# Kernel tuning notes

Measured on AMD Instinct MI355X. Metric: run time of the kernel, lower is better.

## Reference

```python
import jax, jax.numpy as jnp
import numpy as np

B, T, S, NH, MD, FF, H = 2, 4096, 4096, 16, 64, 128, 4
HD = MD // H
NEG_SLOPE = 0.2
MAX_LOG_SCALE = float(np.log(100.0))  # SwinV2-style clamp on learnable logit scale


def layer_norm(x, g, b, eps=1e-5):
    mu = x.mean(-1, keepdims=True)
    var = ((x - mu) ** 2).mean(-1, keepdims=True)
    return (x - mu) * jax.lax.rsqrt(var + eps) * g + b


def leaky(x):
    return jnp.where(x >= 0, x, NEG_SLOPE * x)


def setup_inputs() -> dict:
    key = jax.random.key(0)
    ks = jax.random.split(key, 16)
    p = lambda i, shape: 0.02 * jax.random.normal(ks[i], shape, jnp.float32)
    return dict(
        x=jax.random.normal(ks[0], (B, S, 1), jnp.float32),
        coords_target=jax.random.uniform(ks[1], (B, T, 2), jnp.float32),
        coords_source=jax.random.uniform(ks[2], (B, S, 2), jnp.float32),
        pe_w1=p(3, (2, FF)), pe_b1=jnp.zeros((FF,), jnp.float32),
        pe_w2=p(4, (FF, MD)), pe_b2=jnp.zeros((MD,), jnp.float32),
        q_w=p(5, (MD, MD)), k_w=p(6, (MD, MD)), v_w=p(7, (1, MD)),
        logit_scale=jnp.zeros((H,), jnp.float32),
        out_w=p(8, (MD, MD)), out_b=jnp.zeros((MD,), jnp.float32),
        nh_w1=p(9, (MD, FF)), nh_b1=jnp.zeros((FF,), jnp.float32),
        nh_w2=p(10, (FF, 1)), nh_b2=jnp.zeros((1,), jnp.float32),
        uf_w1=p(11, (MD * NH, MD * NH)), uf_b1=jnp.zeros((MD * NH,), jnp.float32),
        uf_w2=p(12, (MD * NH, MD * NH)), uf_b2=jnp.zeros((MD * NH,), jnp.float32),
        ln1_g=jnp.ones((MD,), jnp.float32), ln1_b=jnp.zeros((MD,), jnp.float32),
        ln2_g=jnp.ones((MD,), jnp.float32), ln2_b=jnp.zeros((MD,), jnp.float32),
        ln3_g=jnp.ones((MD * NH,), jnp.float32), ln3_b=jnp.zeros((MD * NH,), jnp.float32),
    )


def reference(x, coords_target, coords_source, pe_w1, pe_b1, pe_w2, pe_b2,
              q_w, k_w, v_w, logit_scale, out_w, out_b,
              nh_w1, nh_b1, nh_w2, nh_b2, uf_w1, uf_b1, uf_w2, uf_b2,
              ln1_g, ln1_b, ln2_g, ln2_b, ln3_g, ln3_b):
    # ---- nn_layer: kNN gather of source values per target point ----
    d2 = jnp.sum((coords_target[:, :, None, :] - coords_source[:, None, :, :]) ** 2, -1)  # (B,T,S)
    _, idx = jax.lax.top_k(-d2, NH)  # (B,T,NH) nearest source indices
    gather = jax.vmap(lambda a, i: a[i])
    x_nh = gather(x, idx)                  # (B,T,NH,1)
    cs_nh = gather(coords_source, idx)     # (B,T,NH,2)
    rel = cs_nh - coords_target[:, :, None, :]  # relative coords (B,T,NH,2)

    # ---- relative position embedding MLP (with coordinate transform) ----
    c = jnp.sign(rel) * jnp.log1p(jnp.abs(rel))
    pe = jax.nn.relu(c @ pe_w1 + pe_b1) @ pe_w2 + pe_b2  # (B,T,NH,MD)

    # ---- value projection from raw gathered values (before pe add) ----
    v = x_nh.reshape(B * T, NH, 1) @ v_w  # (BT,NH,MD)

    h = layer_norm(x_nh + pe, ln1_g, ln1_b).reshape(B * T, NH, MD)
    q = h @ q_w
    k = h @ k_w

    # ---- local multi-head attention over the NH neighbors (cosine att w/ learnable logit scale) ----
    qh = q.reshape(B * T, NH, H, HD)
    kh = k.reshape(B * T, NH, H, HD)
    vh = v.reshape(B * T, NH, H, HD)
    qn = qh / (jnp.linalg.norm(qh, axis=-1, keepdims=True) + 1e-12)
    kn = kh / (jnp.linalg.norm(kh, axis=-1, keepdims=True) + 1e-12)
    scale = jnp.exp(jnp.minimum(logit_scale, MAX_LOG_SCALE))  # (H,)
    logits = jnp.einsum('nihd,njhd->nhij', qn, kn) * scale[None, :, None, None]
    att = jax.nn.softmax(logits, axis=-1)
    ao = jnp.einsum('nhij,njhd->nihd', att, vh).reshape(B * T, NH, MD)
    ao = ao @ out_w + out_b

    h = layer_norm(h + ao, ln2_g, ln2_b)
    # per-neighborhood MLP: md -> ff -> 1, broadcast residual add
    m = leaky(leaky(h @ nh_w1 + nh_b1) @ nh_w2 + nh_b2)  # (BT,NH,1)
    h = h + m

    # unfold neighbors into channel dim and run wide MLP
    hu = layer_norm(h.reshape(B, T, NH * MD), ln3_g, ln3_b)
    out = leaky(leaky(hu @ uf_w1 + uf_b1) @ uf_w2 + uf_b2)  # (B,T,NH*MD)
    return out
```

## Files before the change

### kernel.cpp

```cpp
#include <hip/hip_runtime.h>
#include <math.h>

#define B_ 2
#define T_ 4096
#define S_ 4096
#define NH_ 16
#define MD_ 64
#define FF_ 128
#define H_ 4
#define HD_ 16
#define BT_ (B_*T_)

typedef unsigned short u16;
typedef unsigned int u32;
typedef unsigned long long u64;
typedef __attribute__((ext_vector_type(8))) short short8;
typedef __attribute__((ext_vector_type(4))) float f32x4;

__device__ __forceinline__ float wsum64(float v) {
  #pragma unroll
  for (int off = 32; off > 0; off >>= 1) v += __shfl_xor(v, off, 64);
  return v;
}
__device__ __forceinline__ float leaky_(float x) { return x >= 0.f ? x : 0.2f * x; }
__device__ __forceinline__ u16 f2bf(float f) {
  u32 u = __float_as_uint(f);
  return (u16)((u + 0x7fffu + ((u >> 16) & 1u)) >> 16);
}
__device__ __forceinline__ float bf2f(u16 h) { return __uint_as_float((u32)h << 16); }

__device__ __forceinline__ void gload16(const void* g, void* l) {
  __builtin_amdgcn_global_load_lds(
      (const __attribute__((address_space(1))) u32*)g,
      (__attribute__((address_space(3))) u32*)l, 16, 0, 0);
}

__device__ __forceinline__ float dist2_(float2 c, float ctx, float cty) {
  float dx = ctx - c.x, dy = cty - c.y;
  return dx * dx + dy * dy;
}

__global__ __launch_bounds__(256) void k1_knn(
    const float* __restrict__ coords_target, const float* __restrict__ coords_source,
    const float* __restrict__ x, float* __restrict__ xnh, float* __restrict__ rel) {
  __shared__ float2 cs_s[S_];
  __shared__ u64 buf[4][128];
  const int tid = threadIdx.x;
  const int lane = tid & 63;
  const int wave = tid >> 6;
  const int n = blockIdx.x * 4 + wave;
  const int b = n >> 12;
  const float2* cs = (const float2*)coords_source + (size_t)b * S_;
  for (int i = tid; i < S_; i += 256) cs_s[i] = cs[i];
  __syncthreads();

  const float ctx = coords_target[n*2+0], cty = coords_target[n*2+1];

  float lmin = INFINITY;
  for (int kk = 0; kk < 64; ++kk)
    lmin = fminf(lmin, dist2_(cs_s[(kk << 6) | lane], ctx, cty));

  float v = lmin;
  #pragma unroll
  for (int k = 2; k <= 64; k <<= 1) {
    #pragma unroll
    for (int j = k >> 1; j > 0; j >>= 1) {
      float o = __shfl_xor(v, j, 64);
      bool keepmin = (((lane & j) == 0) == ((lane & k) == 0));
      v = keepmin ? fminf(v, o) : fmaxf(v, o);
    }
  }
  const float tau = __shfl(v, 15, 64);

  u64* wbuf = buf[wave];
  int cnt = 0;
  for (int kk = 0; kk < 64; ++kk) {
    int s = (kk << 6) | lane;
    float d2 = dist2_(cs_s[s], ctx, cty);
    bool q = (d2 <= tau);
    u64 mask = __ballot(q);
    if (q) {
      int pos = cnt + __popcll(mask & ((1ull << lane) - 1ull));
      if (pos < 128)
        wbuf[pos] = ((u64)__float_as_uint(d2) << 32) | (u32)s;
    }
    cnt += (int)__popcll(mask);
  }

  int myidx = 0;
  if (cnt >= 16 && cnt <= 128) {
    u64 c0 = (lane < cnt) ? wbuf[lane] : ~0ull;
    u64 c1 = (lane + 64 < cnt) ? wbuf[lane + 64] : ~0ull;
    for (int r = 0; r < 16; ++r) {
      u64 m = c0 < c1 ? c0 : c1;
      #pragma unroll
      for (int off = 32; off > 0; off >>= 1) {
        u64 o = __shfl_xor(m, off, 64);
        m = o < m ? o : m;
      }
      if (lane == r) myidx = (int)(u32)(m & 0xffffffffu);
      if (c0 == m) c0 = ~0ull;
      else if (c1 == m) c1 = ~0ull;
    }
  } else {
    float kd[16]; int ki[16];
    #pragma unroll
    for (int j = 0; j < 16; ++j) { kd[j] = INFINITY; ki[j] = 0x7fffffff; }
    for (int kk = 0; kk < 64; ++kk) {
      int s = (kk << 6) | lane;
      float d2 = dist2_(cs_s[s], ctx, cty);
      if (d2 < kd[15]) {
        float cd = d2; int ci = s;
        #pragma unroll
        for (int j = 0; j < 16; ++j) {
          bool sw = cd < kd[j];
          float td = sw ? kd[j] : cd;  int ti = sw ? ki[j] : ci;
          kd[j]    = sw ? cd : kd[j];  ki[j]    = sw ? ci : ki[j];
          cd = td; ci = ti;
        }
      }
    }
    for (int r = 0; r < 16; ++r) {
      float hd = kd[0]; int hi = ki[0];
      #pragma unroll
      for (int off = 32; off > 0; off >>= 1) {
        float od = __shfl_xor(hd, off, 64); int oi = __shfl_xor(hi, off, 64);
        bool take = (od < hd) || (od == hd && oi < hi);
        hd = take ? od : hd; hi = take ? oi : hi;
      }
      if (kd[0] == hd && ki[0] == hi) {
        #pragma unroll
        for (int j = 0; j < 15; ++j) { kd[j] = kd[j+1]; ki[j] = ki[j+1]; }
        kd[15] = INFINITY; ki[15] = 0x7fffffff;
      }
      if (lane == r) myidx = hi;
    }
  }

  if (lane < 16) {
    float2 c = cs_s[myidx];
    xnh[(size_t)n*NH_ + lane] = x[(size_t)b*S_ + myidx];
    rel[((size_t)n*NH_ + lane)*2 + 0] = c.x - ctx;
    rel[((size_t)n*NH_ + lane)*2 + 1] = c.y - cty;
  }
}

__global__ __launch_bounds__(256) void k2_pe(
    const float* __restrict__ rel, const float* __restrict__ xnh,
    const float* __restrict__ pe_w1, const float* __restrict__ pe_b1,
    const float* __restrict__ pe_w2, const float* __restrict__ pe_b2,
    const float* __restrict__ ln1_g, const float* __restrict__ ln1_b,
    float* __restrict__ h_out) {
  const int lane = threadIdx.x & 63;
  const int wave = threadIdx.x >> 6;
  __shared__ float hid[4][4][128];
  const int row0 = blockIdx.x * 16 + wave * 4;

  float c0[4], c1[4], xn[4];
  #pragma unroll
  for (int rr = 0; rr < 4; ++rr) {
    int row = row0 + rr;
    float r0 = rel[(size_t)row*2+0], r1 = rel[(size_t)row*2+1];
    float a0 = log1pf(fabsf(r0)), a1 = log1pf(fabsf(r1));
    c0[rr] = r0 > 0.f ? a0 : (r0 < 0.f ? -a0 : 0.f);
    c1[rr] = r1 > 0.f ? a1 : (r1 < 0.f ? -a1 : 0.f);
    xn[rr] = xnh[row];
  }
  const float w1a0 = pe_w1[lane],    w1a1 = pe_w1[128+lane], b1a = pe_b1[lane];
  const float w1b0 = pe_w1[64+lane], w1b1 = pe_w1[192+lane], b1b = pe_b1[64+lane];
  #pragma unroll
  for (int rr = 0; rr < 4; ++rr) {
    hid[wave][rr][lane]    = fmaxf(fmaf(c0[rr], w1a0, fmaf(c1[rr], w1a1, b1a)), 0.f);
    hid[wave][rr][lane+64] = fmaxf(fmaf(c0[rr], w1b0, fmaf(c1[rr], w1b1, b1b)), 0.f);
  }
  __syncthreads();

  const float b2 = pe_b2[lane];
  float acc[4] = {b2, b2, b2, b2};
  for (int j = 0; j < 128; ++j) {
    float w2 = pe_w2[(size_t)j*64 + lane];
    #pragma unroll
    for (int rr = 0; rr < 4; ++rr) acc[rr] = fmaf(hid[wave][rr][j], w2, acc[rr]);
  }

  const float g = ln1_g[lane], bb = ln1_b[lane];
  #pragma unroll
  for (int rr = 0; rr < 4; ++rr) {
    float v = xn[rr] + acc[rr];
    float mu = wsum64(v) * (1.f/64.f);
    float d = v - mu;
    float var = wsum64(d*d) * (1.f/64.f);
    h_out[(size_t)(row0+rr)*64 + lane] = d * rsqrtf(var + 1e-5f) * g + bb;
  }
}

#define HBF_S 72
#define QKS2 24
__global__ __launch_bounds__(256) void k3_attn(
    const float* __restrict__ h_in, const float* __restrict__ xnh,
    const u16* __restrict__ qkwt_hi, const u16* __restrict__ qkwt_lo,
    const u16* __restrict__ nhw1t_hi, const u16* __restrict__ nhw1t_lo,
    const float* __restrict__ v_w, const float* __restrict__ logit_scale,
    const float* __restrict__ out_w, const float* __restrict__ out_b,
    const float* __restrict__ nh_b1, const float* __restrict__ nh_w2,
    const float* __restrict__ nh_b2,
    const float* __restrict__ ln2_g, const float* __restrict__ ln2_b,
    const float* __restrict__ ln3_g, const float* __restrict__ ln3_b,
    u16* __restrict__ hu_hi, u16* __restrict__ hu_lo) {
  const int tid = threadIdx.x;
  const int lane = tid & 63;
  const int wave = tid >> 6;
  const int n = blockIdx.x * 4 + wave;

  __shared__ u16 h_bf[2][64][HBF_S];
  __shared__ u16 q_s[4][64][QKS2];
  __shared__ u16 k_s[4][64][QKS2];
  __shared__ float xnh_s[64];
  __shared__ float svx_s[4][16][4];
  __shared__ float mred[4][64];

  const float* hb = h_in + (size_t)n * (NH_*MD_);
  float hr[16];
  #pragma unroll
  for (int i = 0; i < 16; ++i) {
    hr[i] = hb[i*64 + lane];
    u16 hi16 = f2bf(hr[i]);
    h_bf[0][wave*16 + i][lane] = hi16;
    h_bf[1][wave*16 + i][lane] = f2bf(hr[i] - bf2f(hi16));
  }
  if (tid < 64) xnh_s[tid] = xnh[(size_t)blockIdx.x * 64 + tid];

  float wvo[4];
  #pragma unroll
  for (int h = 0; h < 4; ++h) {
    float a = 0.f;
    for (int d = 0; d < 16; ++d)
      a = fmaf(v_w[h*16+d], out_w[(size_t)(h*16+d)*64 + lane], a);
    wvo[h] = a;
  }
  __syncthreads();

  const int fr = lane & 15, fq = lane >> 4;
  {
    short8 bqh[2], bql[2], bkh[2], bkl[2];
    #pragma unroll
    for (int ks = 0; ks < 2; ++ks) {
      const int qcol = wave*16 + fr, kcol = 64 + wave*16 + fr;
      const int ko = ks*32 + fq*8;
      bqh[ks] = *(const short8*)&qkwt_hi[qcol*64 + ko];
      bql[ks] = *(const short8*)&qkwt_lo[qcol*64 + ko];
      bkh[ks] = *(const short8*)&qkwt_hi[kcol*64 + ko];
      bkl[ks] = *(const short8*)&qkwt_lo[kcol*64 + ko];
    }
    f32x4 accq[4], acck[4];
    #pragma unroll
    for (int mf = 0; mf < 4; ++mf) { accq[mf] = (f32x4){0,0,0,0}; acck[mf] = (f32x4){0,0,0,0}; }
    #pragma unroll
    for (int ks = 0; ks < 2; ++ks) {
      #pragma unroll
      for (int mf = 0; mf < 4; ++mf) {
        short8 ah = *(const short8*)&h_bf[0][mf*16 + fr][ks*32 + fq*8];
        short8 al = *(const short8*)&h_bf[1][mf*16 + fr][ks*32 + fq*8];
        accq[mf] = __builtin_amdgcn_mfma_f32_16x16x32_bf16(ah, bqh[ks], accq[mf], 0,0,0);
        accq[mf] = __builtin_amdgcn_mfma_f32_16x16x32_bf16(ah, bql[ks], accq[mf], 0,0,0);
        accq[mf] = __builtin_amdgcn_mfma_f32_16x16x32_bf16(al, bqh[ks], accq[mf], 0,0,0);
        acck[mf] = __builtin_amdgcn_mfma_f32_16x16x32_bf16(ah, bkh[ks], acck[mf], 0,0,0);
        acck[mf] = __builtin_amdgcn_mfma_f32_16x16x32_bf16(ah, bkl[ks], acck[mf], 0,0,0);
        acck[mf] = __builtin_amdgcn_mfma_f32_16x16x32_bf16(al, bkh[ks], acck[mf], 0,0,0);
      }
    }
    #pragma unroll
    for (int mf = 0; mf < 4; ++mf)
      #pragma unroll
      for (int r = 0; r < 4; ++r) {
        const int row = mf*16 + fq*4 + r;
        q_s[wave][row][fr] = f2bf(accq[mf][r]);
        k_s[wave][row][fr] = f2bf(acck[mf][r]);
      }
  }
  __syncthreads();

  {
    const int nl = lane >> 4, il = lane & 15;
    const float sc = expf(fminf(logit_scale[wave], 4.60517019f));
    float qv[16]; float qs = 0.f;
    short8 qp0 = *(const short8*)&q_s[wave][lane][0];
    short8 qp1 = *(const short8*)&q_s[wave][lane][8];
    #pragma unroll
    for (int d = 0; d < 8; ++d) {
      qv[d]   = bf2f((u16)qp0[d]);  qs = fmaf(qv[d],   qv[d],   qs);
      qv[8+d] = bf2f((u16)qp1[d]);  qs = fmaf(qv[8+d], qv[8+d], qs);
    }
    const float rq = 1.f / (sqrtf(qs) + 1e-12f);
    float lg[16];
    #pragma unroll
    for (int j = 0; j < 16; ++j) {
      short8 kp0 = *(const short8*)&k_s[wave][(lane & 48) + j][0];
      short8 kp1 = *(const short8*)&k_s[wave][(lane & 48) + j][8];
      float ks = 0.f, dt = 0.f;
      #pragma unroll
      for (int d = 0; d < 8; ++d) {
        float kv0 = bf2f((u16)kp0[d]);
        float kv1 = bf2f((u16)kp1[d]);
        ks = fmaf(kv0, kv0, ks); dt = fmaf(qv[d], kv0, dt);
        ks = fmaf(kv1, kv1, ks); dt = fmaf(qv[8+d], kv1, dt);
      }
      lg[j] = dt * rq * (1.f/(sqrtf(ks)+1e-12f)) * sc;
    }
    float mx = lg[0];
    #pragma unroll
    for (int j = 1; j < 16; ++j) mx = fmaxf(mx, lg[j]);
    float se = 0.f, sx = 0.f;
    #pragma unroll
    for (int j = 0; j < 16; ++j) {
      float e = __expf(lg[j] - mx);
      se += e;
      sx = fmaf(e, xnh_s[(lane & 48) + j], sx);
    }
    svx_s[nl][il][wave] = sx / se;
  }
  __syncthreads();

  const float ob = out_b[lane], g2 = ln2_g[lane], bb2 = ln2_b[lane];
  float h2[16];
  #pragma unroll
  for (int i = 0; i < 16; ++i) {
    float o = ob;
    #pragma unroll
    for (int h = 0; h < 4; ++h) o = fmaf(svx_s[wave][i][h], wvo[h], o);
    float t = hr[i] + o;
    float mu = wsum64(t) * (1.f/64.f);
    float d = t - mu;
    float var = wsum64(d*d) * (1.f/64.f);
    h2[i] = d * rsqrtf(var + 1e-5f) * g2 + bb2;
  }
  #pragma unroll
  for (int i = 0; i < 16; ++i) {
    u16 hi16 = f2bf(h2[i]);
    h_bf[0][wave*16 + i][lane] = hi16;
    h_bf[1][wave*16 + i][lane] = f2bf(h2[i] - bf2f(hi16));
  }
  __syncthreads();

  {
    short8 bnh[2][2], bnl[2][2];
    float b1v[2], w2v[2];
    #pragma unroll
    for (int cf = 0; cf < 2; ++cf) {
      const int col = wave*32 + cf*16 + fr;
      b1v[cf] = nh_b1[col];
      w2v[cf] = nh_w2[col];
      #pragma unroll
      for (int ks = 0; ks < 2; ++ks) {
        bnh[cf][ks] = *(const short8*)&nhw1t_hi[col*64 + ks*32 + fq*8];
        bnl[cf][ks] = *(const short8*)&nhw1t_lo[col*64 + ks*32 + fq*8];
      }
    }
    f32x4 accm[4][2];
    #pragma unroll
    for (int mf = 0; mf < 4; ++mf)
      #pragma unroll
      for (int cf = 0; cf < 2; ++cf) accm[mf][cf] = (f32x4){0,0,0,0};
    #pragma unroll
    for (int ks = 0; ks < 2; ++ks) {
      #pragma unroll
      for (int mf = 0; mf < 4; ++mf) {
        short8 ah = *(const short8*)&h_bf[0][mf*16 + fr][ks*32 + fq*8];
        short8 al = *(const short8*)&h_bf[1][mf*16 + fr][ks*32 + fq*8];
        #pragma unroll
        for (int cf = 0; cf < 2; ++cf) {
          accm[mf][cf] = __builtin_amdgcn_mfma_f32_16x16x32_bf16(ah, bnh[cf][ks], accm[mf][cf], 0,0,0);
          accm[mf][cf] = __builtin_amdgcn_mfma_f32_16x16x32_bf16(ah, bnl[cf][ks], accm[mf][cf], 0,0,0);
          accm[mf][cf] = __builtin_amdgcn_mfma_f32_16x16x32_bf16(al, bnh[cf][ks], accm[mf][cf], 0,0,0);
        }
      }
    }
    #pragma unroll
    for (int mf = 0; mf < 4; ++mf)
      #pragma unroll
      for (int r = 0; r < 4; ++r) {
        float p = leaky_(accm[mf][0][r] + b1v[0]) * w2v[0]
                + leaky_(accm[mf][1][r] + b1v[1]) * w2v[1];
        #pragma unroll
        for (int off = 1; off < 16; off <<= 1) p += __shfl_xor(p, off, 64);
        if (fr == 0) mred[wave][mf*16 + fq*4 + r] = p;
      }
  }
  __syncthreads();

  const float nb2 = nh_b2[0];
  float s1 = 0.f, s2 = 0.f;
  #pragma unroll
  for (int i = 0; i < 16; ++i) {
    float sm = mred[0][wave*16+i] + mred[1][wave*16+i]
             + mred[2][wave*16+i] + mred[3][wave*16+i];
    float mi = leaky_(sm + nb2);
    float v3 = h2[i] + mi;
    hr[i] = v3;
    s1 += v3; s2 = fmaf(v3, v3, s2);
  }
  s1 = wsum64(s1); s2 = wsum64(s2);
  float mu = s1 * (1.f/1024.f);
  float var = s2 * (1.f/1024.f) - mu*mu;
  float rs = rsqrtf(var + 1e-5f);
  const size_t base = (size_t)n * 1024;
  #pragma unroll
  for (int i = 0; i < 16; ++i) {
    int cch = i*64 + lane;
    float v = (hr[i] - mu) * rs * ln3_g[cch] + ln3_b[cch];
    u16 hi16 = f2bf(v);
    hu_hi[base + cch] = hi16;
    hu_lo[base + cch] = f2bf(v - bf2f(hi16));
  }
}

__global__ __launch_bounds__(256) void k0_wsplit(
    const float* __restrict__ W1, const float* __restrict__ W2,
    u16* __restrict__ T1h, u16* __restrict__ T1l,
    u16* __restrict__ T2h, u16* __restrict__ T2l) {
  __shared__ float t[64][65];
  const float* W = blockIdx.z ? W2 : W1;
  u16* Th = blockIdx.z ? T2h : T1h;
  u16* Tl = blockIdx.z ? T2l : T1l;
  const int bx = blockIdx.x * 64, by = blockIdx.y * 64;
  for (int i = threadIdx.x; i < 64*64; i += 256) {
    int r = i >> 6, c = i & 63;
    t[r][c] = W[(size_t)(bx + r) * 1024 + by + c];
  }
  __syncthreads();
  for (int i = threadIdx.x; i < 64*64; i += 256) {
    int r2 = i >> 6, c2 = i & 63;
    float v = t[c2][r2];
    u16 hi = f2bf(v);
    size_t o = (size_t)(by + r2) * 1024 + bx + c2;
    Th[o] = hi;
    Tl[o] = f2bf(v - bf2f(hi));
  }
}

__global__ __launch_bounds__(256) void k0b_wsplit2(
    const float* __restrict__ q_w, const float* __restrict__ k_w,
    const float* __restrict__ nh_w1,
    u16* __restrict__ qkwt_hi, u16* __restrict__ qkwt_lo,
    u16* __restrict__ nhw1t_hi, u16* __restrict__ nhw1t_lo) {
  int idx = blockIdx.x * 256 + threadIdx.x;
  int e = idx & 8191;
  int col = e >> 6, kk = e & 63;
  if (idx < 8192) {
    float v = (col < 64) ? q_w[kk*64 + col] : k_w[kk*64 + (col - 64)];
    u16 hi = f2bf(v);
    qkwt_hi[col*64 + kk] = hi;
    qkwt_lo[col*64 + kk] = f2bf(v - bf2f(hi));
  } else {
    float v = nh_w1[kk*128 + col];
    u16 hi = f2bf(v);
    nhw1t_hi[col*64 + kk] = hi;
    nhw1t_lo[col*64 + kk] = f2bf(v - bf2f(hi));
  }
}

template<int OUT_BF16>
__global__ __launch_bounds__(256, 2) void k5_gemm(
    const u16* __restrict__ Ah, const u16* __restrict__ Al,
    const u16* __restrict__ Bth, const u16* __restrict__ Btl,
    const float* __restrict__ bias,
    u16* __restrict__ Chi, u16* __restrict__ Clo, float* __restrict__ Cf) {
  __shared__ u16 As[2][128*32];
  __shared__ u16 Bs[2][128*32];
  const int tid = threadIdx.x;
  const int lane = tid & 63;
  const int wave = tid >> 6;
  const int wr = (wave >> 1) * 64, wc = (wave & 1) * 64;
  const int mt = (int)blockIdx.x >> 3, nt = (int)blockIdx.x & 7;
  const int m0 = mt * 128, n0 = nt * 128;

  const int sr = tid >> 2, sk = (tid & 3) * 8;
  const size_t a_off = (size_t)(m0 + sr) * 1024 + sk;
  const size_t b_off = (size_t)(n0 + sr) * 1024 + sk;
  u16* lAh = &As[0][0] + tid * 8;
  u16* lAl = &As[1][0] + tid * 8;
  u16* lBh = &Bs[0][0] + tid * 8;
  u16* lBl = &Bs[1][0] + tid * 8;

  f32x4 acc[4][4];
  #pragma unroll
  for (int i = 0; i < 4; ++i)
    #pragma unroll
    for (int j = 0; j < 4; ++j) acc[i][j] = (f32x4){0.f, 0.f, 0.f, 0.f};

  const int fr = lane & 15, fq = lane >> 4;
  const int aoff = (wr + fr) * 32 + fq * 8;
  const int boff = (wc + fr) * 32 + fq * 8;

  for (int k0 = 0; k0 < 1024; k0 += 32) {
    __syncthreads();
    gload16(Ah  + a_off + k0,             lAh);
    gload16(Ah  + a_off + k0 + 64*1024,   lAh + 64*32);
    gload16(Al  + a_off + k0,             lAl);
    gload16(Al  + a_off + k0 + 64*1024,   lAl + 64*32);
    gload16(Bth + b_off + k0,             lBh);
    gload16(Bth + b_off + k0 + 64*1024,   lBh + 64*32);
    gload16(Btl + b_off + k0,             lBl);
    gload16(Btl + b_off + k0 + 64*1024,   lBl + 64*32);
    __syncthreads();

    short8 ah[4], al[4], bh[4], bl[4];
    #pragma unroll
    for (int i = 0; i < 4; ++i) {
      ah[i] = *(const short8*)&As[0][aoff + i*16*32];
      al[i] = *(const short8*)&As[1][aoff + i*16*32];
      bh[i] = *(const short8*)&Bs[0][boff + i*16*32];
      bl[i] = *(const short8*)&Bs[1][boff + i*16*32];
    }
    #pragma unroll
    for (int mi = 0; mi < 4; ++mi)
      #pragma unroll
      for (int ni = 0; ni < 4; ++ni) {
        acc[mi][ni] = __builtin_amdgcn_mfma_f32_16x16x32_bf16(ah[mi], bh[ni], acc[mi][ni], 0, 0, 0);
        acc[mi][ni] = __builtin_amdgcn_mfma_f32_16x16x32_bf16(ah[mi], bl[ni], acc[mi][ni], 0, 0, 0);
        acc[mi][ni] = __builtin_amdgcn_mfma_f32_16x16x32_bf16(al[mi], bh[ni], acc[mi][ni], 0, 0, 0);
      }
  }

  #pragma unroll
  for (int mi = 0; mi < 4; ++mi)
    #pragma unroll
    for (int ni = 0; ni < 4; ++ni) {
      const int col = n0 + wc + ni*16 + fr;
      const float bv = bias[col];
      #pragma unroll
      for (int r = 0; r < 4; ++r) {
        const int row = m0 + wr + mi*16 + fq*4 + r;
        float v = leaky_(acc[mi][ni][r] + bv);
        if (OUT_BF16) {
          u16 hi = f2bf(v);
          Chi[(size_t)row*1024 + col] = hi;
          Clo[(size_t)row*1024 + col] = f2bf(v - bf2f(hi));
        } else {
          Cf[(size_t)row*1024 + col] = v;
        }
      }
    }
}

extern "C" void kernel_launch(void* const* d_in, const int* in_sizes, int n_in,
                              void* d_out, int out_size, void* d_ws, size_t ws_size,
                              hipStream_t stream) {
  (void)in_sizes; (void)n_in; (void)out_size; (void)ws_size;
  const float* x     = (const float*)d_in[0];
  const float* ct    = (const float*)d_in[1];
  const float* cs    = (const float*)d_in[2];
  const float* pe_w1 = (const float*)d_in[3];
  const float* pe_b1 = (const float*)d_in[4];
  const float* pe_w2 = (const float*)d_in[5];
  const float* pe_b2 = (const float*)d_in[6];
  const float* q_w   = (const float*)d_in[7];
  const float* k_w   = (const float*)d_in[8];
  const float* v_w   = (const float*)d_in[9];
  const float* lsc   = (const float*)d_in[10];
  const float* out_w = (const float*)d_in[11];
  const float* out_b = (const float*)d_in[12];
  const float* nh_w1 = (const float*)d_in[13];
  const float* nh_b1 = (const float*)d_in[14];
  const float* nh_w2 = (const float*)d_in[15];
  const float* nh_b2 = (const float*)d_in[16];
  const float* uf_w1 = (const float*)d_in[17];
  const float* uf_b1 = (const float*)d_in[18];
  const float* uf_w2 = (const float*)d_in[19];
  const float* uf_b2 = (const float*)d_in[20];
  const float* ln1_g = (const float*)d_in[21];
  const float* ln1_b = (const float*)d_in[22];
  const float* ln2_g = (const float*)d_in[23];
  const float* ln2_b = (const float*)d_in[24];
  const float* ln3_g = (const float*)d_in[25];
  const float* ln3_b = (const float*)d_in[26];

  float* ws  = (float*)d_ws;
  float* xnh = ws;
  float* rel = ws + 131072;
  float* h   = ws + 393216;
  u16*  hu_hi = (u16*)(ws + 393216 + 8388608);
  u16*  hu_lo = hu_hi + 8388608;
  u16*  wbase = (u16*)(ws + 393216 + 2*8388608);
  u16*  w1t_hi = wbase;
  u16*  w1t_lo = wbase + 1048576;
  u16*  w2t_hi = wbase + 2*1048576;
  u16*  w2t_lo = wbase + 3*1048576;
  u16*  qkwt_hi  = wbase + 4*1048576;
  u16*  qkwt_lo  = qkwt_hi + 8192;
  u16*  nhw1t_hi = qkwt_hi + 16384;
  u16*  nhw1t_lo = qkwt_hi + 24576;
  u16*  mid_hi = (u16*)h;
  u16*  mid_lo = mid_hi + 8388608;
  float* out = (float*)d_out;

  k0_wsplit<<<dim3(16, 16, 2), dim3(256), 0, stream>>>(uf_w1, uf_w2,
                                                       w1t_hi, w1t_lo, w2t_hi, w2t_lo);
  k0b_wsplit2<<<dim3(64), dim3(256), 0, stream>>>(q_w, k_w, nh_w1,
                                                  qkwt_hi, qkwt_lo, nhw1t_hi, nhw1t_lo);
  k1_knn<<<dim3(BT_/4), dim3(256), 0, stream>>>(ct, cs, x, xnh, rel);
  k2_pe<<<dim3(BT_*NH_/16), dim3(256), 0, stream>>>(rel, xnh, pe_w1, pe_b1, pe_w2, pe_b2,
                                                    ln1_g, ln1_b, h);
  k3_attn<<<dim3(BT_/4), dim3(256), 0, stream>>>(h, xnh, qkwt_hi, qkwt_lo,
                                                 nhw1t_hi, nhw1t_lo,
                                                 v_w, lsc, out_w, out_b,
                                                 nh_b1, nh_w2, nh_b2,
                                                 ln2_g, ln2_b, ln3_g, ln3_b, hu_hi, hu_lo);
  k5_gemm<1><<<dim3(512), dim3(256), 0, stream>>>(hu_hi, hu_lo, w1t_hi, w1t_lo, uf_b1,
                                                  mid_hi, mid_lo, nullptr);
  k5_gemm<0><<<dim3(512), dim3(256), 0, stream>>>(mid_hi, mid_lo, w2t_hi, w2t_lo, uf_b2,
                                                  nullptr, nullptr, out);
}
```

Measured before the change: 466.5 us.

## Fuse positional-encoding MLP and LN1 into attention kernel using split-bf16 MFMA

```diff
diff --git a/kernel.cpp b/kernel.cpp
--- a/kernel.cpp
+++ b/kernel.cpp
@@ -145,59 +145,14 @@
   }
 }
 
-__global__ __launch_bounds__(256) void k2_pe(
-    const float* __restrict__ rel, const float* __restrict__ xnh,
-    const float* __restrict__ pe_w1, const float* __restrict__ pe_b1,
-    const float* __restrict__ pe_w2, const float* __restrict__ pe_b2,
-    const float* __restrict__ ln1_g, const float* __restrict__ ln1_b,
-    float* __restrict__ h_out) {
-  const int lane = threadIdx.x & 63;
-  const int wave = threadIdx.x >> 6;
-  __shared__ float hid[4][4][128];
-  const int row0 = blockIdx.x * 16 + wave * 4;
-
-  float c0[4], c1[4], xn[4];
-  #pragma unroll
-  for (int rr = 0; rr < 4; ++rr) {
-    int row = row0 + rr;
-    float r0 = rel[(size_t)row*2+0], r1 = rel[(size_t)row*2+1];
-    float a0 = log1pf(fabsf(r0)), a1 = log1pf(fabsf(r1));
-    c0[rr] = r0 > 0.f ? a0 : (r0 < 0.f ? -a0 : 0.f);
-    c1[rr] = r1 > 0.f ? a1 : (r1 < 0.f ? -a1 : 0.f);
-    xn[rr] = xnh[row];
-  }
-  const float w1a0 = pe_w1[lane],    w1a1 = pe_w1[128+lane], b1a = pe_b1[lane];
-  const float w1b0 = pe_w1[64+lane], w1b1 = pe_w1[192+lane], b1b = pe_b1[64+lane];
-  #pragma unroll
-  for (int rr = 0; rr < 4; ++rr) {
-    hid[wave][rr][lane]    = fmaxf(fmaf(c0[rr], w1a0, fmaf(c1[rr], w1a1, b1a)), 0.f);
-    hid[wave][rr][lane+64] = fmaxf(fmaf(c0[rr], w1b0, fmaf(c1[rr], w1b1, b1b)), 0.f);
-  }
-  __syncthreads();
-
-  const float b2 = pe_b2[lane];
-  float acc[4] = {b2, b2, b2, b2};
-  for (int j = 0; j < 128; ++j) {
-    float w2 = pe_w2[(size_t)j*64 + lane];
-    #pragma unroll
-    for (int rr = 0; rr < 4; ++rr) acc[rr] = fmaf(hid[wave][rr][j], w2, acc[rr]);
-  }
-
-  const float g = ln1_g[lane], bb = ln1_b[lane];
-  #pragma unroll
-  for (int rr = 0; rr < 4; ++rr) {
-    float v = xn[rr] + acc[rr];
-    float mu = wsum64(v) * (1.f/64.f);
-    float d = v - mu;
-    float var = wsum64(d*d) * (1.f/64.f);
-    h_out[(size_t)(row0+rr)*64 + lane] = d * rsqrtf(var + 1e-5f) * g + bb;
-  }
-}
-
 #define HBF_S 72
 #define QKS2 24
 __global__ __launch_bounds__(256) void k3_attn(
-    const float* __restrict__ h_in, const float* __restrict__ xnh,
+    const float* __restrict__ rel, const float* __restrict__ xnh,
+    const float* __restrict__ pe_w1, const float* __restrict__ pe_b1,
+    const u16* __restrict__ pew2t_hi, const u16* __restrict__ pew2t_lo,
+    const float* __restrict__ pe_b2,
+    const float* __restrict__ ln1_g, const float* __restrict__ ln1_b,
     const u16* __restrict__ qkwt_hi, const u16* __restrict__ qkwt_lo,
     const u16* __restrict__ nhw1t_hi, const u16* __restrict__ nhw1t_lo,
     const float* __restrict__ v_w, const float* __restrict__ logit_scale,
@@ -211,25 +166,28 @@
   const int lane = tid & 63;
   const int wave = tid >> 6;
   const int n = blockIdx.x * 4 + wave;
-
-  __shared__ u16 h_bf[2][64][HBF_S];
-  __shared__ u16 q_s[4][64][QKS2];
-  __shared__ u16 k_s[4][64][QKS2];
-  __shared__ float xnh_s[64];
-  __shared__ float svx_s[4][16][4];
-  __shared__ float mred[4][64];
-
-  const float* hb = h_in + (size_t)n * (NH_*MD_);
-  float hr[16];
-  #pragma unroll
-  for (int i = 0; i < 16; ++i) {
-    hr[i] = hb[i*64 + lane];
-    u16 hi16 = f2bf(hr[i]);
-    h_bf[0][wave*16 + i][lane] = hi16;
-    h_bf[1][wave*16 + i][lane] = f2bf(hr[i] - bf2f(hi16));
-  }
-  if (tid < 64) xnh_s[tid] = xnh[(size_t)blockIdx.x * 64 + tid];
-
+  const int fr = lane & 15, fq = lane >> 4;
+
+  __shared__ __align__(16) char smem[45824];
+  u16* h_bf0 = (u16*)smem;
+  u16* h_bf1 = h_bf0 + 64*HBF_S;
+  u16* qkreg = h_bf1 + 64*HBF_S;
+  u16* q_sB  = qkreg;
+  u16* k_sB  = qkreg + 4*64*QKS2;
+  u16* hid0  = qkreg;
+  u16* hid1  = qkreg + 64*HBF_S;
+  float* fmisc = (float*)(qkreg + 8*64*QKS2);
+  float* xnh_s = fmisc;
+  float* svx_s = fmisc + 64;
+  float* mred  = fmisc + 64 + 256;
+  float* c_s   = fmisc + 64 + 256 + 256;
+
+  if (lane < 32) {
+    float rv = rel[(size_t)blockIdx.x*128 + wave*32 + lane];
+    float a = log1pf(fabsf(rv));
+    c_s[wave*32 + lane] = rv > 0.f ? a : (rv < 0.f ? -a : 0.f);
+  }
+  if (tid < 64) xnh_s[tid] = xnh[(size_t)blockIdx.x*64 + tid];
   float wvo[4];
   #pragma unroll
   for (int h = 0; h < 4; ++h) {
@@ -240,7 +198,74 @@
   }
   __syncthreads();
 
-  const int fr = lane & 15, fq = lane >> 4;
+  f32x4 acc_pe[4];
+  #pragma unroll
+  for (int nf = 0; nf < 4; ++nf) acc_pe[nf] = (f32x4){0,0,0,0};
+  for (int p = 0; p < 2; ++p) {
+    const float w10 = pe_w1[p*64 + lane];
+    const float w11 = pe_w1[128 + p*64 + lane];
+    const float b1  = pe_b1[p*64 + lane];
+    #pragma unroll
+    for (int i = 0; i < 16; ++i) {
+      float c0 = c_s[wave*32 + i*2], c1v = c_s[wave*32 + i*2 + 1];
+      float hv = fmaxf(fmaf(c0, w10, fmaf(c1v, w11, b1)), 0.f);
+      u16 hh = f2bf(hv);
+      hid0[(wave*16+i)*HBF_S + lane] = hh;
+      hid1[(wave*16+i)*HBF_S + lane] = f2bf(hv - bf2f(hh));
+    }
+    __syncthreads();
+    #pragma unroll
+    for (int ks = 0; ks < 2; ++ks) {
+      short8 ah = *(const short8*)&hid0[(wave*16+fr)*HBF_S + ks*32 + fq*8];
+      short8 al = *(const short8*)&hid1[(wave*16+fr)*HBF_S + ks*32 + fq*8];
+      #pragma unroll
+      for (int nf = 0; nf < 4; ++nf) {
+        short8 bh = *(const short8*)&pew2t_hi[(nf*16+fr)*128 + p*64 + ks*32 + fq*8];
+        short8 bl = *(const short8*)&pew2t_lo[(nf*16+fr)*128 + p*64 + ks*32 + fq*8];
+        acc_pe[nf] = __builtin_amdgcn_mfma_f32_16x16x32_bf16(ah, bh, acc_pe[nf], 0,0,0);
+        acc_pe[nf] = __builtin_amdgcn_mfma_f32_16x16x32_bf16(ah, bl, acc_pe[nf], 0,0,0);
+        acc_pe[nf] = __builtin_amdgcn_mfma_f32_16x16x32_bf16(al, bh, acc_pe[nf], 0,0,0);
+      }
+    }
+    __syncthreads();
+  }
+
+  {
+    float gv[4], bv[4], b2v[4];
+    #pragma unroll
+    for (int nf = 0; nf < 4; ++nf) {
+      int ch = nf*16 + fr;
+      gv[nf] = ln1_g[ch]; bv[nf] = ln1_b[ch]; b2v[nf] = pe_b2[ch];
+    }
+    #pragma unroll
+    for (int r = 0; r < 4; ++r) {
+      const int row = wave*16 + fq*4 + r;
+      const float xv = xnh_s[row];
+      float t[4];
+      #pragma unroll
+      for (int nf = 0; nf < 4; ++nf) t[nf] = acc_pe[nf][r] + b2v[nf] + xv;
+      float ps = t[0]+t[1]+t[2]+t[3];
+      #pragma unroll
+      for (int off = 1; off < 16; off <<= 1) ps += __shfl_xor(ps, off, 64);
+      float mu = ps * (1.f/64.f);
+      float vs = 0.f;
+      #pragma unroll
+      for (int nf = 0; nf < 4; ++nf) { float d = t[nf]-mu; vs = fmaf(d,d,vs); }
+      #pragma unroll
+      for (int off = 1; off < 16; off <<= 1) vs += __shfl_xor(vs, off, 64);
+      float rs = rsqrtf(vs*(1.f/64.f) + 1e-5f);
+      #pragma unroll
+      for (int nf = 0; nf < 4; ++nf) {
+        int ch = nf*16 + fr;
+        float hn = (t[nf]-mu)*rs*gv[nf] + bv[nf];
+        u16 hh = f2bf(hn);
+        h_bf0[row*HBF_S + ch] = hh;
+        h_bf1[row*HBF_S + ch] = f2bf(hn - bf2f(hh));
+      }
+    }
+  }
+  __syncthreads();
+
   {
     short8 bqh[2], bql[2], bkh[2], bkl[2];
     #pragma unroll
@@ -259,8 +284,8 @@
     for (int ks = 0; ks < 2; ++ks) {
       #pragma unroll
       for (int mf = 0; mf < 4; ++mf) {
-        short8 ah = *(const short8*)&h_bf[0][mf*16 + fr][ks*32 + fq*8];
-        short8 al = *(const short8*)&h_bf[1][mf*16 + fr][ks*32 + fq*8];
+        short8 ah = *(const short8*)&h_bf0[(mf*16+fr)*HBF_S + ks*32 + fq*8];
+        short8 al = *(const short8*)&h_bf1[(mf*16+fr)*HBF_S + ks*32 + fq*8];
         accq[mf] = __builtin_amdgcn_mfma_f32_16x16x32_bf16(ah, bqh[ks], accq[mf], 0,0,0);
         accq[mf] = __builtin_amdgcn_mfma_f32_16x16x32_bf16(ah, bql[ks], accq[mf], 0,0,0);
         accq[mf] = __builtin_amdgcn_mfma_f32_16x16x32_bf16(al, bqh[ks], accq[mf], 0,0,0);
@@ -274,8 +299,8 @@
       #pragma unroll
       for (int r = 0; r < 4; ++r) {
         const int row = mf*16 + fq*4 + r;
-        q_s[wave][row][fr] = f2bf(accq[mf][r]);
-        k_s[wave][row][fr] = f2bf(acck[mf][r]);
+        q_sB[(wave*64+row)*QKS2 + fr] = f2bf(accq[mf][r]);
+        k_sB[(wave*64+row)*QKS2 + fr] = f2bf(acck[mf][r]);
       }
   }
   __syncthreads();
@@ -284,8 +309,8 @@
     const int nl = lane >> 4, il = lane & 15;
     const float sc = expf(fminf(logit_scale[wave], 4.60517019f));
     float qv[16]; float qs = 0.f;
-    short8 qp0 = *(const short8*)&q_s[wave][lane][0];
-    short8 qp1 = *(const short8*)&q_s[wave][lane][8];
+    short8 qp0 = *(const short8*)&q_sB[(wave*64+lane)*QKS2 + 0];
+    short8 qp1 = *(const short8*)&q_sB[(wave*64+lane)*QKS2 + 8];
     #pragma unroll
     for (int d = 0; d < 8; ++d) {
       qv[d]   = bf2f((u16)qp0[d]);  qs = fmaf(qv[d],   qv[d],   qs);
@@ -295,8 +320,9 @@
     float lg[16];
     #pragma unroll
     for (int j = 0; j < 16; ++j) {
-      short8 kp0 = *(const short8*)&k_s[wave][(lane & 48) + j][0];
-      short8 kp1 = *(const short8*)&k_s[wave][(lane & 48) + j][8];
+      const int krow = (lane & 48) + j;
+      short8 kp0 = *(const short8*)&k_sB[(wave*64+krow)*QKS2 + 0];
+      short8 kp1 = *(const short8*)&k_sB[(wave*64+krow)*QKS2 + 8];
       float ks = 0.f, dt = 0.f;
       #pragma unroll
       for (int d = 0; d < 8; ++d) {
@@ -317,7 +343,7 @@
       se += e;
       sx = fmaf(e, xnh_s[(lane & 48) + j], sx);
     }
-    svx_s[nl][il][wave] = sx / se;
+    svx_s[(nl*16 + il)*4 + wave] = sx / se;
   }
   __syncthreads();
 
@@ -325,20 +351,19 @@
   float h2[16];
   #pragma unroll
   for (int i = 0; i < 16; ++i) {
+    float hfull = bf2f(h_bf0[(wave*16+i)*HBF_S + lane])
+                + bf2f(h_bf1[(wave*16+i)*HBF_S + lane]);
     float o = ob;
     #pragma unroll
-    for (int h = 0; h < 4; ++h) o = fmaf(svx_s[wave][i][h], wvo[h], o);
-    float t = hr[i] + o;
+    for (int h = 0; h < 4; ++h) o = fmaf(svx_s[(wave*16+i)*4 + h], wvo[h], o);
+    float t = hfull + o;
     float mu = wsum64(t) * (1.f/64.f);
     float d = t - mu;
     float var = wsum64(d*d) * (1.f/64.f);
     h2[i] = d * rsqrtf(var + 1e-5f) * g2 + bb2;
-  }
-  #pragma unroll
-  for (int i = 0; i < 16; ++i) {
-    u16 hi16 = f2bf(h2[i]);
-    h_bf[0][wave*16 + i][lane] = hi16;
-    h_bf[1][wave*16 + i][lane] = f2bf(h2[i] - bf2f(hi16));
+    u16 hh = f2bf(h2[i]);
+    h_bf0[(wave*16+i)*HBF_S + lane] = hh;
+    h_bf1[(wave*16+i)*HBF_S + lane] = f2bf(h2[i] - bf2f(hh));
   }
   __syncthreads();
 
@@ -365,8 +390,8 @@
     for (int ks = 0; ks < 2; ++ks) {
       #pragma unroll
       for (int mf = 0; mf < 4; ++mf) {
-        short8 ah = *(const short8*)&h_bf[0][mf*16 + fr][ks*32 + fq*8];
-        short8 al = *(const short8*)&h_bf[1][mf*16 + fr][ks*32 + fq*8];
+        short8 ah = *(const short8*)&h_bf0[(mf*16+fr)*HBF_S + ks*32 + fq*8];
+        short8 al = *(const short8*)&h_bf1[(mf*16+fr)*HBF_S + ks*32 + fq*8];
         #pragma unroll
         for (int cf = 0; cf < 2; ++cf) {
           accm[mf][cf] = __builtin_amdgcn_mfma_f32_16x16x32_bf16(ah, bnh[cf][ks], accm[mf][cf], 0,0,0);
@@ -383,20 +408,21 @@
                 + leaky_(accm[mf][1][r] + b1v[1]) * w2v[1];
         #pragma unroll
         for (int off = 1; off < 16; off <<= 1) p += __shfl_xor(p, off, 64);
-        if (fr == 0) mred[wave][mf*16 + fq*4 + r] = p;
+        if (fr == 0) mred[wave*64 + mf*16 + fq*4 + r] = p;
       }
   }
   __syncthreads();
 
   const float nb2 = nh_b2[0];
+  float h3[16];
   float s1 = 0.f, s2 = 0.f;
   #pragma unroll
   for (int i = 0; i < 16; ++i) {
-    float sm = mred[0][wave*16+i] + mred[1][wave*16+i]
-             + mred[2][wave*16+i] + mred[3][wave*16+i];
+    float sm = mred[0*64 + wave*16+i] + mred[1*64 + wave*16+i]
+             + mred[2*64 + wave*16+i] + mred[3*64 + wave*16+i];
     float mi = leaky_(sm + nb2);
     float v3 = h2[i] + mi;
-    hr[i] = v3;
+    h3[i] = v3;
     s1 += v3; s2 = fmaf(v3, v3, s2);
   }
   s1 = wsum64(s1); s2 = wsum64(s2);
@@ -407,7 +433,7 @@
   #pragma unroll
   for (int i = 0; i < 16; ++i) {
     int cch = i*64 + lane;
-    float v = (hr[i] - mu) * rs * ln3_g[cch] + ln3_b[cch];
+    float v = (h3[i] - mu) * rs * ln3_g[cch] + ln3_b[cch];
     u16 hi16 = f2bf(v);
     hu_hi[base + cch] = hi16;
     hu_lo[base + cch] = f2bf(v - bf2f(hi16));
@@ -440,22 +466,31 @@
 
 __global__ __launch_bounds__(256) void k0b_wsplit2(
     const float* __restrict__ q_w, const float* __restrict__ k_w,
-    const float* __restrict__ nh_w1,
+    const float* __restrict__ nh_w1, const float* __restrict__ pe_w2,
     u16* __restrict__ qkwt_hi, u16* __restrict__ qkwt_lo,
-    u16* __restrict__ nhw1t_hi, u16* __restrict__ nhw1t_lo) {
+    u16* __restrict__ nhw1t_hi, u16* __restrict__ nhw1t_lo,
+    u16* __restrict__ pew2t_hi, u16* __restrict__ pew2t_lo) {
   int idx = blockIdx.x * 256 + threadIdx.x;
-  int e = idx & 8191;
-  int col = e >> 6, kk = e & 63;
   if (idx < 8192) {
+    int col = idx >> 6, kk = idx & 63;
     float v = (col < 64) ? q_w[kk*64 + col] : k_w[kk*64 + (col - 64)];
     u16 hi = f2bf(v);
     qkwt_hi[col*64 + kk] = hi;
     qkwt_lo[col*64 + kk] = f2bf(v - bf2f(hi));
-  } else {
+  } else if (idx < 16384) {
+    int e = idx - 8192;
+    int col = e >> 6, kk = e & 63;
     float v = nh_w1[kk*128 + col];
     u16 hi = f2bf(v);
     nhw1t_hi[col*64 + kk] = hi;
     nhw1t_lo[col*64 + kk] = f2bf(v - bf2f(hi));
+  } else {
+    int e = idx - 16384;
+    int col = e >> 7, j = e & 127;
+    float v = pe_w2[j*64 + col];
+    u16 hi = f2bf(v);
+    pew2t_hi[col*128 + j] = hi;
+    pew2t_lo[col*128 + j] = f2bf(v - bf2f(hi));
   }
 }
 
@@ -471,7 +506,9 @@
   const int lane = tid & 63;
   const int wave = tid >> 6;
   const int wr = (wave >> 1) * 64, wc = (wave & 1) * 64;
-  const int mt = (int)blockIdx.x >> 3, nt = (int)blockIdx.x & 7;
+  const int bid = (int)blockIdx.x;
+  const int swz = (bid & 7) * 64 + (bid >> 3);
+  const int mt = swz >> 3, nt = swz & 7;
   const int m0 = mt * 128, n0 = nt * 128;
 
   const int sr = tid >> 2, sk = (tid & 3) * 8;
@@ -590,19 +627,22 @@
   u16*  qkwt_lo  = qkwt_hi + 8192;
   u16*  nhw1t_hi = qkwt_hi + 16384;
   u16*  nhw1t_lo = qkwt_hi + 24576;
+  u16*  pew2t_hi = qkwt_hi + 32768;
+  u16*  pew2t_lo = qkwt_hi + 40960;
   u16*  mid_hi = (u16*)h;
   u16*  mid_lo = mid_hi + 8388608;
   float* out = (float*)d_out;
 
   k0_wsplit<<<dim3(16, 16, 2), dim3(256), 0, stream>>>(uf_w1, uf_w2,
                                                        w1t_hi, w1t_lo, w2t_hi, w2t_lo);
-  k0b_wsplit2<<<dim3(64), dim3(256), 0, stream>>>(q_w, k_w, nh_w1,
-                                                  qkwt_hi, qkwt_lo, nhw1t_hi, nhw1t_lo);
+  k0b_wsplit2<<<dim3(96), dim3(256), 0, stream>>>(q_w, k_w, nh_w1, pe_w2,
+                                                  qkwt_hi, qkwt_lo, nhw1t_hi, nhw1t_lo,
+                                                  pew2t_hi, pew2t_lo);
   k1_knn<<<dim3(BT_/4), dim3(256), 0, stream>>>(ct, cs, x, xnh, rel);
-  k2_pe<<<dim3(BT_*NH_/16), dim3(256), 0, stream>>>(rel, xnh, pe_w1, pe_b1, pe_w2, pe_b2,
-                                                    ln1_g, ln1_b, h);
-  k3_attn<<<dim3(BT_/4), dim3(256), 0, stream>>>(h, xnh, qkwt_hi, qkwt_lo,
-                                                 nhw1t_hi, nhw1t_lo,
+  k3_attn<<<dim3(BT_/4), dim3(256), 0, stream>>>(rel, xnh, pe_w1, pe_b1,
+                                                 pew2t_hi, pew2t_lo, pe_b2,
+                                                 ln1_g, ln1_b,
+                                                 qkwt_hi, qkwt_lo, nhw1t_hi, nhw1t_lo,
                                                  v_w, lsc, out_w, out_b,
                                                  nh_b1, nh_w2, nh_b2,
                                                  ln2_g, ln2_b, ln3_g, ln3_b, hu_hi, hu_lo);
```

New measurement: 428.3 us. 8.2% less time.
